# Kernel tuning notes

Measured on AMD Instinct MI355X. Metric: run time of the kernel, lower is better.

Reference implementation:

```python
import jax, jax.numpy as jnp
import numpy as np

N, E, D = 50000, 800000, 64  # nodes, edges, feature dim (all feature dims must match, see module)
EPS = 1e-5


def _linear_params(key, fin, fout):
    k1, k2 = jax.random.split(key)
    s = 1.0 / np.sqrt(fin)
    W = jax.random.uniform(k1, (fout, fin), minval=-s, maxval=s, dtype=jnp.float32)
    b = jax.random.uniform(k2, (fout,), minval=-s, maxval=s, dtype=jnp.float32)
    return W, b


def setup_inputs() -> dict:
    key = jax.random.key(0)
    ks = jax.random.split(key, 9)
    h = jax.random.normal(ks[0], (N, D), dtype=jnp.float32)
    e = jax.random.normal(ks[1], (E, D), dtype=jnp.float32)
    src = jax.random.randint(ks[2], (E,), 0, N)
    dst = jax.random.randint(ks[3], (E,), 0, N)
    W_upd, b_upd = _linear_params(ks[4], 3 * D, D)   # upd_linear: cat(h_src,h_dst,e) -> D
    W_act, b_act = _linear_params(ks[5], D, D)       # activation_linear
    W_gd, b_gd = _linear_params(ks[6], D, D)         # gating_dst_linear
    W_gs, b_gs = _linear_params(ks[7], D, D)         # gating_src_linear
    W_out, b_out = _linear_params(ks[8], D, D)       # final linear
    g_un = jnp.ones((D,), jnp.float32); be_un = jnp.zeros((D,), jnp.float32)  # upd_norm gamma/beta
    g_gn = jnp.ones((D,), jnp.float32); be_gn = jnp.zeros((D,), jnp.float32)  # gating_norm gamma/beta
    return dict(h=h, e=e, src=src, dst=dst,
                W_upd=W_upd, b_upd=b_upd, g_un=g_un, be_un=be_un,
                W_act=W_act, b_act=b_act, W_gd=W_gd, b_gd=b_gd,
                W_gs=W_gs, b_gs=b_gs, g_gn=g_gn, be_gn=be_gn,
                W_out=W_out, b_out=b_out)


def _batchnorm(x, gamma, beta):
    # nn.BatchNorm1d in training mode: biased batch stats over axis 0
    m = x.mean(axis=0)
    v = x.var(axis=0)
    return (x - m) * jax.lax.rsqrt(v + EPS) * gamma + beta


def reference(h, e, src, dst, W_upd, b_upd, g_un, be_un, W_act, b_act,
              W_gd, b_gd, W_gs, b_gs, g_gn, be_gn, W_out, b_out):
    n_nodes = h.shape[0]
    # --- edge update: gather endpoints, linear, batchnorm, SiLU, residual ---
    e_cat = jnp.concatenate([h[src], h[dst], e], axis=1)       # [E, 3D]
    e_lin = e_cat @ W_upd.T + b_upd                             # [E, D]
    e2 = e + jax.nn.silu(_batchnorm(e_lin, g_un, be_un))        # residual (dims equal)
    # --- edge softmax grouped by destination node ---
    logit = e2 @ W_act.T + b_act                                # [E, D]
    mx = jax.ops.segment_max(logit, dst, num_segments=n_nodes)  # [N, D]
    ex = jnp.exp(logit - mx[dst])
    den = jax.ops.segment_sum(ex, dst, num_segments=n_nodes)
    a = ex / den[dst]                                           # [E, D]
    # --- gated aggregation: mail = a * W_gd h_dst, scatter-sum to dst ---
    mail = a * (h[dst] @ W_gd.T + b_gd)                         # [E, D]
    agg = jax.ops.segment_sum(mail, dst, num_segments=n_nodes)  # [N, D]
    h2 = (h @ W_gs.T + b_gs) + agg
    h2 = jax.nn.silu(_batchnorm(h2, g_gn, be_gn)) + h
    h2 = h2 @ W_out.T + b_out
    return (h2, e2)
```

## Files before the change

kernel.cpp:

```cpp
#include <hip/hip_runtime.h>

#define N_NODES 50000
#define N_EDGES 800000
#define EPS_BN 1e-5f
#define EBLK (N_EDGES / 128)
#define NBLK ((N_NODES + 127) / 128)


typedef __attribute__((ext_vector_type(8))) short s16x8;
typedef __attribute__((ext_vector_type(4))) float f32x4;

__device__ __forceinline__ unsigned short f2bf(float f) {
  unsigned int u = __float_as_uint(f);
  u += 0x7FFFu + ((u >> 16) & 1u);
  return (unsigned short)(u >> 16);
}
__device__ __forceinline__ unsigned int pack2(float lo, float hi) {
  return (unsigned int)f2bf(lo) | ((unsigned int)f2bf(hi) << 16);
}
__device__ __forceinline__ s16x8 cvt8(float4 a, float4 b) {
  union { s16x8 v; unsigned int u[4]; } r;
  r.u[0] = pack2(a.x, a.y); r.u[1] = pack2(a.z, a.w);
  r.u[2] = pack2(b.x, b.y); r.u[3] = pack2(b.z, b.w);
  return r.v;
}
__device__ __forceinline__ float siluf(float x) { return x / (1.f + __expf(-x)); }

__global__ void k_pre(unsigned int* __restrict__ wsu,
                      const float* __restrict__ W_upd, const float* __restrict__ W_gd,
                      const float* __restrict__ W_gs, const float* __restrict__ W_out,
                      const float* __restrict__ h, short* __restrict__ hbf) {
  int b = blockIdx.x;
  if (b < 49) {
    int i = b * 256 + threadIdx.x;
    if (i < 512) wsu[i] = 0u;
    if (i < 12500) wsu[12800 + i] = 0u;
    if (i < 6144) {
      int s = i >> 2, w = i & 3;
      int row = s / 24, slot = s - row * 24;
      int ii = slot ^ (row & 7);
      int fidx = row * 192 + ii * 8 + w * 2;
      wsu[512 + i] = pack2(W_upd[fidx], W_upd[fidx + 1]);
    }
    if (i < 2048) {
      float2 a = *(const float2*)&W_gd[(size_t)i * 2];
      float2 bb = *(const float2*)&W_gs[(size_t)i * 2];
      float2 c = *(const float2*)&W_out[(size_t)i * 2];
      wsu[6656 + i] = pack2(a.x, a.y);
      wsu[8704 + i] = pack2(bb.x, bb.y);
      wsu[10752 + i] = pack2(c.x, c.y);
    }
  } else {
    int t = (b - 49) * 256 + threadIdx.x;
    if (t < (N_NODES * 64) / 8) {
      float4 a = *(const float4*)&h[(size_t)t * 8];
      float4 bb = *(const float4*)&h[(size_t)t * 8 + 4];
      *(s16x8*)&hbf[(size_t)t * 8] = cvt8(a, bb);
    }
  }
}

template<int PHASE>
__global__ __launch_bounds__(256, PHASE == 0 ? 5 : 4) void k_edge(
    const short* __restrict__ hbf, const float* __restrict__ e,
    const int* __restrict__ src, const int* __restrict__ dst,
    const unsigned int* __restrict__ wsu, const float* __restrict__ b_upd,
    const float* __restrict__ ws, unsigned char* __restrict__ flb,
    const float* __restrict__ b_gd, const float* __restrict__ b_gs,
    float* __restrict__ wsm, float* __restrict__ v_out,
    float* __restrict__ out_e)
{
  __shared__ short Bls[64 * 192];
  __shared__ float red[4][128];

  int tid = threadIdx.x;
  int ln = tid & 63, wv = tid >> 6;
  int lr = ln & 15, lq = ln >> 4, lk = lq * 8;

  if (PHASE == 1 && blockIdx.x < NBLK) {
    short* Bgd = Bls;
    short* Bgs = Bls + 4096;
    const uint4* Sgd = (const uint4*)(wsu + 6656);
    const uint4* Sgs = (const uint4*)(wsu + 8704);
    #pragma unroll
    for (int j = 0; j < 2; ++j) {
      int c = tid + j * 256;
      int row = c >> 3, i = c & 7, sl = row * 8 + (i ^ (row & 7));
      ((uint4*)Bgd)[sl] = Sgd[c];
      ((uint4*)Bgs)[sl] = Sgs[c];
    }
    int n0 = blockIdx.x * 128;
    int r0 = wv * 32 + lr, r1 = r0 + 16;
    int nA = min(n0 + r0, N_NODES - 1), nB = min(n0 + r1, N_NODES - 1);
    s16x8 A0[2], A1[2];
    A0[0] = *(const s16x8*)&hbf[nA * 64 + lk];
    A0[1] = *(const s16x8*)&hbf[nA * 64 + 32 + lk];
    A1[0] = *(const s16x8*)&hbf[nB * 64 + lk];
    A1[1] = *(const s16x8*)&hbf[nB * 64 + 32 + lk];
    __syncthreads();

    f32x4 zero4 = {0.f, 0.f, 0.f, 0.f};
    f32x4 accd[2][4], accs[2][4];
    #pragma unroll
    for (int rt = 0; rt < 2; ++rt)
      #pragma unroll
      for (int ct = 0; ct < 4; ++ct) { accd[rt][ct] = zero4; accs[rt][ct] = zero4; }
    #pragma unroll
    for (int ct = 0; ct < 4; ++ct) {
      int row = ct * 16 + lr, r7 = row & 7;
      #pragma unroll
      for (int kk = 0; kk < 2; ++kk) {
        int sl = ((kk * 4 + lq) ^ r7) << 3;
        s16x8 bd = *(const s16x8*)&Bgd[row * 64 + sl];
        s16x8 bs = *(const s16x8*)&Bgs[row * 64 + sl];
        accd[0][ct] = __builtin_amdgcn_mfma_f32_16x16x32_bf16(A0[kk], bd, accd[0][ct], 0, 0, 0);
        accd[1][ct] = __builtin_amdgcn_mfma_f32_16x16x32_bf16(A1[kk], bd, accd[1][ct], 0, 0, 0);
        accs[0][ct] = __builtin_amdgcn_mfma_f32_16x16x32_bf16(A0[kk], bs, accs[0][ct], 0, 0, 0);
        accs[1][ct] = __builtin_amdgcn_mfma_f32_16x16x32_bf16(A1[kk], bs, accs[1][ct], 0, 0, 0);
      }
    }
    float s1[4], s2[4];
    #pragma unroll
    for (int ct = 0; ct < 4; ++ct) {
      int col = ct * 16 + lr;
      float bd = b_gd[col], bs = b_gs[col];
      float a1s = 0.f, a2s = 0.f;
      #pragma unroll
      for (int rt = 0; rt < 2; ++rt)
        #pragma unroll
        for (int q = 0; q < 4; ++q) {
          int row = wv * 32 + rt * 16 + lq * 4 + q;
          int n = n0 + row;
          if (n < N_NODES) {
            float fl = (float)flb[n];
            float v = accs[rt][ct][q] + bs + fl * (accd[rt][ct][q] + bd);
            v_out[(size_t)n * 64 + col] = v;
            a1s += v; a2s += v * v;
          }
        }
      s1[ct] = a1s; s2[ct] = a2s;
    }
    #pragma unroll
    for (int ct = 0; ct < 4; ++ct) {
      s1[ct] += __shfl_xor(s1[ct], 16); s1[ct] += __shfl_xor(s1[ct], 32);
      s2[ct] += __shfl_xor(s2[ct], 16); s2[ct] += __shfl_xor(s2[ct], 32);
    }
    if (ln < 16) {
      #pragma unroll
      for (int ct = 0; ct < 4; ++ct) {
        red[wv][ct * 16 + ln] = s1[ct];
        red[wv][64 + ct * 16 + ln] = s2[ct];
      }
    }
    __syncthreads();
    if (tid < 128) {
      float t = red[0][tid] + red[1][tid] + red[2][tid] + red[3][tid];
      atomicAdd(&wsm[256 + tid], t);
    }
    return;
  }

  int ebid = (PHASE == 1) ? (blockIdx.x - NBLK) : blockIdx.x;
  int m0 = ebid * 128;
  int r0 = wv * 32 + lr, r1 = r0 + 16;
  int mA = m0 + r0, mB = m0 + r1;

  const float* pe0 = e + (size_t)mA * 64 + lk;
  const float* pe1 = e + (size_t)mB * 64 + lk;
  float4 e0a = *(const float4*)(pe0);
  float4 e0b = *(const float4*)(pe0 + 4);
  float4 e0c = *(const float4*)(pe0 + 32);
  float4 e0d = *(const float4*)(pe0 + 36);
  float4 e1a = *(const float4*)(pe1);
  float4 e1b = *(const float4*)(pe1 + 4);
  float4 e1c = *(const float4*)(pe1 + 32);
  float4 e1d = *(const float4*)(pe1 + 36);

  int s0 = src[mA], d0 = dst[mA];
  int s1i = src[mB], d1 = dst[mB];

  if (PHASE == 0 && lq == 0) { flb[d0] = 1; flb[d1] = 1; }

  s16x8 A0[6], A1[6];
  A0[0] = *(const s16x8*)&hbf[s0 * 64 + lk];
  A0[1] = *(const s16x8*)&hbf[s0 * 64 + 32 + lk];
  A0[2] = *(const s16x8*)&hbf[d0 * 64 + lk];
  A0[3] = *(const s16x8*)&hbf[d0 * 64 + 32 + lk];
  A1[0] = *(const s16x8*)&hbf[s1i * 64 + lk];
  A1[1] = *(const s16x8*)&hbf[s1i * 64 + 32 + lk];
  A1[2] = *(const s16x8*)&hbf[d1 * 64 + lk];
  A1[3] = *(const s16x8*)&hbf[d1 * 64 + 32 + lk];

  {
    unsigned int* bls32 = (unsigned int*)Bls;
    #pragma unroll
    for (int j = 0; j < 6; ++j) {
      int base = (j * 4 + wv) * 256;
      __builtin_amdgcn_global_load_lds(
          (__attribute__((address_space(1))) void*)(unsigned int*)(wsu + 512 + base + ln * 4),
          (__attribute__((address_space(3))) void*)(bls32 + base),
          16, 0, 0);
    }
  }

  A0[4] = cvt8(e0a, e0b);
  A0[5] = cvt8(e0c, e0d);
  A1[4] = cvt8(e1a, e1b);
  A1[5] = cvt8(e1c, e1d);
  __syncthreads();

  int rl = ln >> 4, c0 = (ln & 15) * 4;
  float4 epre[2][4];
  if (PHASE == 1) {
    #pragma unroll
    for (int rt = 0; rt < 2; ++rt)
      #pragma unroll
      for (int q = 0; q < 4; ++q)
        epre[rt][q] = *(const float4*)&e[(size_t)(m0 + wv * 32 + rt * 16 + rl * 4 + q) * 64 + c0];
  }

  f32x4 zero4 = {0.f, 0.f, 0.f, 0.f};
  f32x4 acc[2][4];
  #pragma unroll
  for (int rt = 0; rt < 2; ++rt)
    #pragma unroll
    for (int ct = 0; ct < 4; ++ct) acc[rt][ct] = zero4;

  #pragma unroll
  for (int ct = 0; ct < 4; ++ct) {
    int row = ct * 16 + lr, r7 = row & 7;
    #pragma unroll
    for (int kk = 0; kk < 6; ++kk) {
      s16x8 b = *(const s16x8*)&Bls[row * 192 + (((kk * 4 + lq) ^ r7) << 3)];
      acc[0][ct] = __builtin_amdgcn_mfma_f32_16x16x32_bf16(A0[kk], b, acc[0][ct], 0, 0, 0);
      acc[1][ct] = __builtin_amdgcn_mfma_f32_16x16x32_bf16(A1[kk], b, acc[1][ct], 0, 0, 0);
    }
  }

  if (PHASE == 0) {
    float s1[4], s2[4];
    #pragma unroll
    for (int ct = 0; ct < 4; ++ct) {
      float bias = b_upd[ct * 16 + lr];
      float a1s = 0.f, a2s = 0.f;
      #pragma unroll
      for (int rt = 0; rt < 2; ++rt)
        #pragma unroll
        for (int q = 0; q < 4; ++q) {
          float v = acc[rt][ct][q] + bias;
          a1s += v; a2s += v * v;
        }
      s1[ct] = a1s; s2[ct] = a2s;
    }
    #pragma unroll
    for (int ct = 0; ct < 4; ++ct) {
      s1[ct] += __shfl_xor(s1[ct], 16); s1[ct] += __shfl_xor(s1[ct], 32);
      s2[ct] += __shfl_xor(s2[ct], 16); s2[ct] += __shfl_xor(s2[ct], 32);
    }
    if (ln < 16) {
      #pragma unroll
      for (int ct = 0; ct < 4; ++ct) {
        red[wv][ct * 16 + ln] = s1[ct];
        red[wv][64 + ct * 16 + ln] = s2[ct];
      }
    }
    __syncthreads();
    if (tid < 128) {
      float t = red[0][tid] + red[1][tid] + red[2][tid] + red[3][tid];
      out_e[(size_t)blockIdx.x * 128 + tid] = t;
    }
  } else {
    #pragma unroll
    for (int ct = 0; ct < 4; ++ct) {
      int col = ct * 16 + lr;
      float scale = ws[128 + col], shift = ws[192 + col], bias = b_upd[col];
      #pragma unroll
      for (int rt = 0; rt < 2; ++rt)
        #pragma unroll
        for (int q = 0; q < 4; ++q) {
          float x = acc[rt][ct][q] + bias;
          acc[rt][ct][q] = siluf(x * scale + shift);
        }
    }
    __syncthreads();
    float* T = (float*)((char*)Bls + wv * 1280);
    #pragma unroll
    for (int rt = 0; rt < 2; ++rt) {
      #pragma unroll
      for (int q = 0; q < 4; ++q) {
        #pragma unroll
        for (int ct = 0; ct < 4; ++ct)
          T[lq * 72 + ct * 16 + lr] = acc[rt][ct][q];
        float4 t4 = *(const float4*)&T[rl * 72 + c0];
        float4 ev = epre[rt][q];
        t4.x += ev.x; t4.y += ev.y; t4.z += ev.z; t4.w += ev.w;
        *(float4*)&out_e[(size_t)(m0 + wv * 32 + rt * 16 + rl * 4 + q) * 64 + c0] = t4;
      }
    }
  }
}

__global__ void k_redfin(const float* __restrict__ partials, float* __restrict__ ws,
                         const float* __restrict__ gamma, const float* __restrict__ beta,
                         float rcount) {
  __shared__ float sr[2][256];
  int c = blockIdx.x;
  float s1 = 0.f, s2 = 0.f;
  for (int i = threadIdx.x; i < EBLK; i += 256) {
    s1 += partials[(size_t)i * 128 + c];
    s2 += partials[(size_t)i * 128 + 64 + c];
  }
  sr[0][threadIdx.x] = s1; sr[1][threadIdx.x] = s2;
  __syncthreads();
  for (int off = 128; off >= 1; off >>= 1) {
    if (threadIdx.x < off) {
      sr[0][threadIdx.x] += sr[0][threadIdx.x + off];
      sr[1][threadIdx.x] += sr[1][threadIdx.x + off];
    }
    __syncthreads();
  }
  if (threadIdx.x == 0) {
    float mean = sr[0][0] * rcount;
    float var = sr[1][0] * rcount - mean * mean;
    float a = rsqrtf(var + EPS_BN) * gamma[c];
    ws[128 + c] = a;
    ws[192 + c] = beta[c] - mean * a;
  }
}

__global__ __launch_bounds__(256, 4) void k_nout(
    const float* __restrict__ h, const unsigned int* __restrict__ wsu,
    const float* __restrict__ g_gn, const float* __restrict__ be_gn,
    const float* __restrict__ b_out, const float* __restrict__ ws,
    const float* __restrict__ v_in, float* __restrict__ out_h)
{
  __shared__ short R1[128 * 64];
  __shared__ short R2[64 * 64];
  __shared__ float sA[64], sB[64];
  int tid = threadIdx.x;
  int ln = tid & 63, wv = tid >> 6;
  int lr = ln & 15, lq = ln >> 4;
  int n0 = blockIdx.x * 128;

  const uint4* Sot = (const uint4*)(wsu + 10752);
  #pragma unroll
  for (int j = 0; j < 2; ++j) {
    int c = tid + j * 256;
    int row = c >> 3, i = c & 7, sl = row * 8 + (i ^ (row & 7));
    ((uint4*)R2)[sl] = Sot[c];
  }
  if (tid < 64) {
    float mean = ws[256 + tid] * (1.f / (float)N_NODES);
    float var = ws[320 + tid] * (1.f / (float)N_NODES) - mean * mean;
    float a = rsqrtf(var + EPS_BN) * g_gn[tid];
    sA[tid] = a;
    sB[tid] = be_gn[tid] - mean * a;
  }
  __syncthreads();

  int c0 = (tid & 15) * 4;
  int rbase = tid >> 4;
  float4 scl = *(const float4*)&sA[c0];
  float4 shf = *(const float4*)&sB[c0];
  #pragma unroll
  for (int i = 0; i < 8; ++i) {
    int row = rbase + 16 * i;
    int n = min(n0 + row, N_NODES - 1);
    float4 v4 = *(const float4*)&v_in[(size_t)n * 64 + c0];
    float4 h4 = *(const float4*)&h[(size_t)n * 64 + c0];
    float tx = siluf(v4.x * scl.x + shf.x) + h4.x;
    float ty = siluf(v4.y * scl.y + shf.y) + h4.y;
    float tz = siluf(v4.z * scl.z + shf.z) + h4.z;
    float tw = siluf(v4.w * scl.w + shf.w) + h4.w;
    int sl = ((((c0 >> 3) ^ (row & 7)) << 3) | (c0 & 7));
    unsigned int* p = (unsigned int*)&R1[row * 64 + sl];
    p[0] = pack2(tx, ty);
    p[1] = pack2(tz, tw);
  }
  __syncthreads();

  int r0 = wv * 32 + lr, r1 = r0 + 16;
  s16x8 T0[2], T1[2];
  #pragma unroll
  for (int kk = 0; kk < 2; ++kk) {
    T0[kk] = *(const s16x8*)&R1[r0 * 64 + (((kk * 4 + lq) ^ (r0 & 7)) << 3)];
    T1[kk] = *(const s16x8*)&R1[r1 * 64 + (((kk * 4 + lq) ^ (r1 & 7)) << 3)];
  }
  f32x4 zero4 = {0.f, 0.f, 0.f, 0.f};
  f32x4 ac2[2][4];
  #pragma unroll
  for (int rt = 0; rt < 2; ++rt)
    #pragma unroll
    for (int ct = 0; ct < 4; ++ct) ac2[rt][ct] = zero4;
  #pragma unroll
  for (int ct = 0; ct < 4; ++ct) {
    int row = ct * 16 + lr, r7 = row & 7;
    #pragma unroll
    for (int kk = 0; kk < 2; ++kk) {
      s16x8 b = *(const s16x8*)&R2[row * 64 + (((kk * 4 + lq) ^ r7) << 3)];
      ac2[0][ct] = __builtin_amdgcn_mfma_f32_16x16x32_bf16(T0[kk], b, ac2[0][ct], 0, 0, 0);
      ac2[1][ct] = __builtin_amdgcn_mfma_f32_16x16x32_bf16(T1[kk], b, ac2[1][ct], 0, 0, 0);
    }
  }
  #pragma unroll
  for (int ct = 0; ct < 4; ++ct) {
    int col = ct * 16 + lr;
    float bo = b_out[col];
    #pragma unroll
    for (int rt = 0; rt < 2; ++rt)
      #pragma unroll
      for (int q = 0; q < 4; ++q) {
        int row = wv * 32 + rt * 16 + lq * 4 + q;
        int n = n0 + row;
        if (n < N_NODES) out_h[(size_t)n * 64 + col] = ac2[rt][ct][q] + bo;
      }
  }
}

extern "C" void kernel_launch(void* const* d_in, const int* in_sizes, int n_in,
                              void* d_out, int out_size, void* d_ws, size_t ws_size,
                              hipStream_t stream) {
  const float* h     = (const float*)d_in[0];
  const float* e     = (const float*)d_in[1];
  const int*   src   = (const int*)d_in[2];
  const int*   dst   = (const int*)d_in[3];
  const float* W_upd = (const float*)d_in[4];
  const float* b_upd = (const float*)d_in[5];
  const float* g_un  = (const float*)d_in[6];
  const float* be_un = (const float*)d_in[7];
  const float* W_gd  = (const float*)d_in[10];
  const float* b_gd  = (const float*)d_in[11];
  const float* W_gs  = (const float*)d_in[12];
  const float* b_gs  = (const float*)d_in[13];
  const float* g_gn  = (const float*)d_in[14];
  const float* be_gn = (const float*)d_in[15];
  const float* W_out = (const float*)d_in[16];
  const float* b_out = (const float*)d_in[17];

  float* outH = (float*)d_out;
  float* outE = outH + (size_t)N_NODES * 64;
  float* ws = (float*)d_ws;
  unsigned int* wsu = (unsigned int*)d_ws;
  unsigned char* flb = (unsigned char*)(wsu + 12800);
  short* hbf = (short*)(wsu + 25600);

  k_pre<<<49 + 1563, 256, 0, stream>>>(wsu, W_upd, W_gd, W_gs, W_out, h, hbf);
  k_edge<0><<<EBLK, 256, 0, stream>>>(hbf, e, src, dst, wsu, b_upd, ws, flb,
                                      nullptr, nullptr, nullptr, nullptr, outH);
  k_redfin<<<64, 256, 0, stream>>>(outH, ws, g_un, be_un, 1.f / (float)N_EDGES);
  k_edge<1><<<NBLK + EBLK, 256, 0, stream>>>(hbf, e, src, dst, wsu, b_upd, ws, flb,
                                             b_gd, b_gs, ws, outH, outE);
  k_nout<<<NBLK, 256, 0, stream>>>(h, wsu, g_gn, be_gn, b_out, ws, outH, outH);
}
```

Measured before the change: 232.8 us.

## Convert edge kernels to persistent grid-stride loops over edge tiles

Both edge-phase kernels now launch a fixed grid of 1024 blocks that loop over 128-edge tiles, instead of one block per tile. The weight tile is loaded into LDS once per block and reused across iterations. Phase-0 batchnorm statistics accumulate in registers across tiles, so there are fewer partials for the reduction kernel to sum. In exchange, each loop iteration serialises gather latency unless multiple waves hide it, the phase-0 occupancy hint drops from 5 to 4, and a separate LDS transpose buffer is added.

```diff
diff --git a/kernel.cpp b/kernel.cpp
--- a/kernel.cpp
+++ b/kernel.cpp
@@ -5,6 +5,7 @@
 #define EPS_BN 1e-5f
 #define EBLK (N_EDGES / 128)
 #define NBLK ((N_NODES + 127) / 128)
+#define EGRID 1024
 
 
 typedef __attribute__((ext_vector_type(8))) short s16x8;
@@ -61,7 +62,7 @@
 }
 
 template<int PHASE>
-__global__ __launch_bounds__(256, PHASE == 0 ? 5 : 4) void k_edge(
+__global__ __launch_bounds__(256, 4) void k_edge(
     const short* __restrict__ hbf, const float* __restrict__ e,
     const int* __restrict__ src, const int* __restrict__ dst,
     const unsigned int* __restrict__ wsu, const float* __restrict__ b_upd,
@@ -71,6 +72,7 @@
     float* __restrict__ out_e)
 {
   __shared__ short Bls[64 * 192];
+  __shared__ float Tq[4][320];
   __shared__ float red[4][128];
 
   int tid = threadIdx.x;
@@ -160,36 +162,7 @@
     return;
   }
 
-  int ebid = (PHASE == 1) ? (blockIdx.x - NBLK) : blockIdx.x;
-  int m0 = ebid * 128;
-  int r0 = wv * 32 + lr, r1 = r0 + 16;
-  int mA = m0 + r0, mB = m0 + r1;
-
-  const float* pe0 = e + (size_t)mA * 64 + lk;
-  const float* pe1 = e + (size_t)mB * 64 + lk;
-  float4 e0a = *(const float4*)(pe0);
-  float4 e0b = *(const float4*)(pe0 + 4);
-  float4 e0c = *(const float4*)(pe0 + 32);
-  float4 e0d = *(const float4*)(pe0 + 36);
-  float4 e1a = *(const float4*)(pe1);
-  float4 e1b = *(const float4*)(pe1 + 4);
-  float4 e1c = *(const float4*)(pe1 + 32);
-  float4 e1d = *(const float4*)(pe1 + 36);
-
-  int s0 = src[mA], d0 = dst[mA];
-  int s1i = src[mB], d1 = dst[mB];
-
-  if (PHASE == 0 && lq == 0) { flb[d0] = 1; flb[d1] = 1; }
-
-  s16x8 A0[6], A1[6];
-  A0[0] = *(const s16x8*)&hbf[s0 * 64 + lk];
-  A0[1] = *(const s16x8*)&hbf[s0 * 64 + 32 + lk];
-  A0[2] = *(const s16x8*)&hbf[d0 * 64 + lk];
-  A0[3] = *(const s16x8*)&hbf[d0 * 64 + 32 + lk];
-  A1[0] = *(const s16x8*)&hbf[s1i * 64 + lk];
-  A1[1] = *(const s16x8*)&hbf[s1i * 64 + 32 + lk];
-  A1[2] = *(const s16x8*)&hbf[d1 * 64 + lk];
-  A1[3] = *(const s16x8*)&hbf[d1 * 64 + 32 + lk];
+  int pb = (PHASE == 1) ? ((int)blockIdx.x - NBLK) : (int)blockIdx.x;
 
   {
     unsigned int* bls32 = (unsigned int*)Bls;
@@ -202,100 +175,131 @@
           16, 0, 0);
     }
   }
-
-  A0[4] = cvt8(e0a, e0b);
-  A0[5] = cvt8(e0c, e0d);
-  A1[4] = cvt8(e1a, e1b);
-  A1[5] = cvt8(e1c, e1d);
   __syncthreads();
 
+  int r0 = wv * 32 + lr, r1 = r0 + 16;
   int rl = ln >> 4, c0 = (ln & 15) * 4;
-  float4 epre[2][4];
-  if (PHASE == 1) {
-    #pragma unroll
-    for (int rt = 0; rt < 2; ++rt)
-      #pragma unroll
-      for (int q = 0; q < 4; ++q)
-        epre[rt][q] = *(const float4*)&e[(size_t)(m0 + wv * 32 + rt * 16 + rl * 4 + q) * 64 + c0];
-  }
-
+  float* T = Tq[wv];
+  float st1[4] = {0.f, 0.f, 0.f, 0.f}, st2[4] = {0.f, 0.f, 0.f, 0.f};
   f32x4 zero4 = {0.f, 0.f, 0.f, 0.f};
-  f32x4 acc[2][4];
-  #pragma unroll
-  for (int rt = 0; rt < 2; ++rt)
-    #pragma unroll
-    for (int ct = 0; ct < 4; ++ct) acc[rt][ct] = zero4;
-
-  #pragma unroll
-  for (int ct = 0; ct < 4; ++ct) {
-    int row = ct * 16 + lr, r7 = row & 7;
-    #pragma unroll
-    for (int kk = 0; kk < 6; ++kk) {
-      s16x8 b = *(const s16x8*)&Bls[row * 192 + (((kk * 4 + lq) ^ r7) << 3)];
-      acc[0][ct] = __builtin_amdgcn_mfma_f32_16x16x32_bf16(A0[kk], b, acc[0][ct], 0, 0, 0);
-      acc[1][ct] = __builtin_amdgcn_mfma_f32_16x16x32_bf16(A1[kk], b, acc[1][ct], 0, 0, 0);
-    }
-  }
-
-  if (PHASE == 0) {
-    float s1[4], s2[4];
-    #pragma unroll
-    for (int ct = 0; ct < 4; ++ct) {
-      float bias = b_upd[ct * 16 + lr];
-      float a1s = 0.f, a2s = 0.f;
+
+  for (int t = pb; t < EBLK; t += EGRID) {
+    int m0 = t * 128;
+    int mA = m0 + r0, mB = m0 + r1;
+
+    const float* pe0 = e + (size_t)mA * 64 + lk;
+    const float* pe1 = e + (size_t)mB * 64 + lk;
+    float4 e0a = *(const float4*)(pe0);
+    float4 e0b = *(const float4*)(pe0 + 4);
+    float4 e0c = *(const float4*)(pe0 + 32);
+    float4 e0d = *(const float4*)(pe0 + 36);
+    float4 e1a = *(const float4*)(pe1);
+    float4 e1b = *(const float4*)(pe1 + 4);
+    float4 e1c = *(const float4*)(pe1 + 32);
+    float4 e1d = *(const float4*)(pe1 + 36);
+
+    int s0 = src[mA], d0 = dst[mA];
+    int s1i = src[mB], d1 = dst[mB];
+    if (PHASE == 0 && lq == 0) { flb[d0] = 1; flb[d1] = 1; }
+
+    s16x8 A0[6], A1[6];
+    A0[0] = *(const s16x8*)&hbf[s0 * 64 + lk];
+    A0[1] = *(const s16x8*)&hbf[s0 * 64 + 32 + lk];
+    A0[2] = *(const s16x8*)&hbf[d0 * 64 + lk];
+    A0[3] = *(const s16x8*)&hbf[d0 * 64 + 32 + lk];
+    A1[0] = *(const s16x8*)&hbf[s1i * 64 + lk];
+    A1[1] = *(const s16x8*)&hbf[s1i * 64 + 32 + lk];
+    A1[2] = *(const s16x8*)&hbf[d1 * 64 + lk];
+    A1[3] = *(const s16x8*)&hbf[d1 * 64 + 32 + lk];
+    A0[4] = cvt8(e0a, e0b);
+    A0[5] = cvt8(e0c, e0d);
+    A1[4] = cvt8(e1a, e1b);
+    A1[5] = cvt8(e1c, e1d);
+
+    float4 epre[2][4];
+    if (PHASE == 1) {
       #pragma unroll
       for (int rt = 0; rt < 2; ++rt)
         #pragma unroll
+        for (int q = 0; q < 4; ++q)
+          epre[rt][q] = *(const float4*)&e[(size_t)(m0 + wv * 32 + rt * 16 + rl * 4 + q) * 64 + c0];
+    }
+
+    f32x4 acc[2][4];
+    #pragma unroll
+    for (int rt = 0; rt < 2; ++rt)
+      #pragma unroll
+      for (int ct = 0; ct < 4; ++ct) acc[rt][ct] = zero4;
+
+    #pragma unroll
+    for (int ct = 0; ct < 4; ++ct) {
+      int row = ct * 16 + lr, r7 = row & 7;
+      #pragma unroll
+      for (int kk = 0; kk < 6; ++kk) {
+        s16x8 b = *(const s16x8*)&Bls[row * 192 + (((kk * 4 + lq) ^ r7) << 3)];
+        acc[0][ct] = __builtin_amdgcn_mfma_f32_16x16x32_bf16(A0[kk], b, acc[0][ct], 0, 0, 0);
+        acc[1][ct] = __builtin_amdgcn_mfma_f32_16x16x32_bf16(A1[kk], b, acc[1][ct], 0, 0, 0);
+      }
+    }
+
+    if (PHASE == 0) {
+      #pragma unroll
+      for (int ct = 0; ct < 4; ++ct) {
+        float bias = b_upd[ct * 16 + lr];
+        #pragma unroll
+        for (int rt = 0; rt < 2; ++rt)
+          #pragma unroll
+          for (int q = 0; q < 4; ++q) {
+            float v = acc[rt][ct][q] + bias;
+            st1[ct] += v; st2[ct] += v * v;
+          }
+      }
+    } else {
+      #pragma unroll
+      for (int ct = 0; ct < 4; ++ct) {
+        int col = ct * 16 + lr;
+        float scale = ws[128 + col], shift = ws[192 + col], bias = b_upd[col];
+        #pragma unroll
+        for (int rt = 0; rt < 2; ++rt)
+          #pragma unroll
+          for (int q = 0; q < 4; ++q) {
+            float x = acc[rt][ct][q] + bias;
+            acc[rt][ct][q] = siluf(x * scale + shift);
+          }
+      }
+      #pragma unroll
+      for (int rt = 0; rt < 2; ++rt) {
+        #pragma unroll
         for (int q = 0; q < 4; ++q) {
-          float v = acc[rt][ct][q] + bias;
-          a1s += v; a2s += v * v;
+          #pragma unroll
+          for (int ct = 0; ct < 4; ++ct)
+            T[lq * 72 + ct * 16 + lr] = acc[rt][ct][q];
+          float4 t4 = *(const float4*)&T[rl * 72 + c0];
+          float4 ev = epre[rt][q];
+          t4.x += ev.x; t4.y += ev.y; t4.z += ev.z; t4.w += ev.w;
+          *(float4*)&out_e[(size_t)(m0 + wv * 32 + rt * 16 + rl * 4 + q) * 64 + c0] = t4;
         }
-      s1[ct] = a1s; s2[ct] = a2s;
-    }
+      }
+    }
+  }
+
+  if (PHASE == 0) {
     #pragma unroll
     for (int ct = 0; ct < 4; ++ct) {
-      s1[ct] += __shfl_xor(s1[ct], 16); s1[ct] += __shfl_xor(s1[ct], 32);
-      s2[ct] += __shfl_xor(s2[ct], 16); s2[ct] += __shfl_xor(s2[ct], 32);
+      st1[ct] += __shfl_xor(st1[ct], 16); st1[ct] += __shfl_xor(st1[ct], 32);
+      st2[ct] += __shfl_xor(st2[ct], 16); st2[ct] += __shfl_xor(st2[ct], 32);
     }
     if (ln < 16) {
       #pragma unroll
       for (int ct = 0; ct < 4; ++ct) {
-        red[wv][ct * 16 + ln] = s1[ct];
-        red[wv][64 + ct * 16 + ln] = s2[ct];
+        red[wv][ct * 16 + ln] = st1[ct];
+        red[wv][64 + ct * 16 + ln] = st2[ct];
       }
     }
     __syncthreads();
     if (tid < 128) {
       float t = red[0][tid] + red[1][tid] + red[2][tid] + red[3][tid];
-      out_e[(size_t)blockIdx.x * 128 + tid] = t;
-    }
-  } else {
-    #pragma unroll
-    for (int ct = 0; ct < 4; ++ct) {
-      int col = ct * 16 + lr;
-      float scale = ws[128 + col], shift = ws[192 + col], bias = b_upd[col];
-      #pragma unroll
-      for (int rt = 0; rt < 2; ++rt)
-        #pragma unroll
-        for (int q = 0; q < 4; ++q) {
-          float x = acc[rt][ct][q] + bias;
-          acc[rt][ct][q] = siluf(x * scale + shift);
-        }
-    }
-    __syncthreads();
-    float* T = (float*)((char*)Bls + wv * 1280);
-    #pragma unroll
-    for (int rt = 0; rt < 2; ++rt) {
-      #pragma unroll
-      for (int q = 0; q < 4; ++q) {
-        #pragma unroll
-        for (int ct = 0; ct < 4; ++ct)
-          T[lq * 72 + ct * 16 + lr] = acc[rt][ct][q];
-        float4 t4 = *(const float4*)&T[rl * 72 + c0];
-        float4 ev = epre[rt][q];
-        t4.x += ev.x; t4.y += ev.y; t4.z += ev.z; t4.w += ev.w;
-        *(float4*)&out_e[(size_t)(m0 + wv * 32 + rt * 16 + rl * 4 + q) * 64 + c0] = t4;
-      }
+      out_e[(size_t)pb * 128 + tid] = t;
     }
   }
 }
@@ -306,7 +310,7 @@
   __shared__ float sr[2][256];
   int c = blockIdx.x;
   float s1 = 0.f, s2 = 0.f;
-  for (int i = threadIdx.x; i < EBLK; i += 256) {
+  for (int i = threadIdx.x; i < EGRID; i += 256) {
     s1 += partials[(size_t)i * 128 + c];
     s2 += partials[(size_t)i * 128 + 64 + c];
   }
@@ -445,10 +449,10 @@
   short* hbf = (short*)(wsu + 25600);
 
   k_pre<<<49 + 1563, 256, 0, stream>>>(wsu, W_upd, W_gd, W_gs, W_out, h, hbf);
-  k_edge<0><<<EBLK, 256, 0, stream>>>(hbf, e, src, dst, wsu, b_upd, ws, flb,
-                                      nullptr, nullptr, nullptr, nullptr, outH);
+  k_edge<0><<<EGRID, 256, 0, stream>>>(hbf, e, src, dst, wsu, b_upd, ws, flb,
+                                       nullptr, nullptr, nullptr, nullptr, outH);
   k_redfin<<<64, 256, 0, stream>>>(outH, ws, g_un, be_un, 1.f / (float)N_EDGES);
-  k_edge<1><<<NBLK + EBLK, 256, 0, stream>>>(hbf, e, src, dst, wsu, b_upd, ws, flb,
-                                             b_gd, b_gs, ws, outH, outE);
+  k_edge<1><<<NBLK + EGRID, 256, 0, stream>>>(hbf, e, src, dst, wsu, b_upd, ws, flb,
+                                              b_gd, b_gs, ws, outH, outE);
   k_nout<<<NBLK, 256, 0, stream>>>(h, wsu, g_gn, be_gn, b_out, ws, outH, outH);
 }
```

After: 445.1 us. 91.2% more time.
